# Kernel tuning notes

Measured on AMD Instinct MI355X. Metric: run time of the kernel, lower is better.

## Reference

```python
import jax, jax.numpy as jnp
import numpy as np

N_HEAD = 16
N_KV_HEADS = 4
HEAD_DIM = 64  # n_emb // n_head = 1024 // 16
WINDOW = 512
NEG_INF = float('-inf')


def _rope_tables(T, dim, dtype):
    inv_freq = 1.0 / (10000.0 ** (jnp.arange(0, dim, 2, dtype=jnp.float32) / dim))
    t = jnp.arange(T, dtype=jnp.float32)
    freqs = jnp.einsum('i,j->ij', t, inv_freq)          # [T, dim/2]
    emb = jnp.concatenate((freqs, freqs), axis=-1)       # [T, dim]
    return jnp.cos(emb).astype(dtype), jnp.sin(emb).astype(dtype)


def _apply_rope(x, cos, sin):
    # x: [B, H, T, D]; cos/sin: [T, D]
    x1, x2 = jnp.split(x, 2, axis=-1)
    x_rot = jnp.concatenate((-x2, x1), axis=-1)
    return x * cos + x_rot * sin


def setup_inputs() -> dict:
    key = jax.random.key(0)
    ks = jax.random.split(key, 5)
    B, T, C = 1, 4096, 1024
    kv_dim = N_KV_HEADS * HEAD_DIM
    s = 0.02
    return {
        'x': jax.random.normal(ks[0], (B, T, C), jnp.float32),
        'wq': jax.random.normal(ks[1], (C, C), jnp.float32) * s,
        'wk': jax.random.normal(ks[2], (kv_dim, C), jnp.float32) * s,
        'wv': jax.random.normal(ks[3], (kv_dim, C), jnp.float32) * s,
        'wo': jax.random.normal(ks[4], (C, C), jnp.float32) * s,
    }


def reference(x, wq, wk, wv, wo):
    B, T, C = x.shape
    n_rep = N_HEAD // N_KV_HEADS
    # QKV projections (torch Linear: x @ W.T)
    q = (x @ wq.T).reshape(B, T, N_HEAD, HEAD_DIM).transpose(0, 2, 1, 3)      # [B,H,T,D]
    k = (x @ wk.T).reshape(B, T, N_KV_HEADS, HEAD_DIM).transpose(0, 2, 1, 3)  # [B,Hkv,T,D]
    v = (x @ wv.T).reshape(B, T, N_KV_HEADS, HEAD_DIM).transpose(0, 2, 1, 3)
    # RoPE
    cos, sin = _rope_tables(T, HEAD_DIM, x.dtype)
    q = _apply_rope(q, cos, sin)
    k = _apply_rope(k, cos, sin)
    # GQA: repeat KV heads
    k = jnp.repeat(k, n_rep, axis=1)  # [B,H,T,D]
    v = jnp.repeat(v, n_rep, axis=1)
    # Sliding-window causal mask: allow j <= i and j > i - WINDOW
    i = jnp.arange(T)[:, None]
    j = jnp.arange(T)[None, :]
    allowed = (j <= i) & (j > i - WINDOW)  # [T,T]
    scale = 1.0 / np.sqrt(HEAD_DIM)
    scores = jnp.einsum('bhqd,bhkd->bhqk', q, k) * scale
    scores = jnp.where(allowed[None, None], scores, NEG_INF)
    attn = jax.nn.softmax(scores, axis=-1)
    y = jnp.einsum('bhqk,bhkd->bhqd', attn, v)            # [B,H,T,D]
    y = y.transpose(0, 2, 1, 3).reshape(B, T, C)
    return y @ wo.T
```

## Files before the change

kernel.cpp:

```cpp
#include <hip/hip_runtime.h>
#include <hip/hip_bf16.h>
#include <stdint.h>

#define T_SEQ 4096
#define CDIM  1024
#define NH    16
#define NKV   4
#define HD    64
#define WIN   512
#define KVD   256
#define QKVN  1536

typedef unsigned short ushort_t;
typedef __attribute__((ext_vector_type(8))) __bf16 bf16x8;
typedef __attribute__((ext_vector_type(4))) float  f32x4;
typedef __attribute__((ext_vector_type(4))) unsigned short us4;

__device__ inline unsigned short f2bf(float f) {
  unsigned u = __builtin_bit_cast(unsigned, f);
  u += 0x7fffu + ((u >> 16) & 1u);
  return (unsigned short)(u >> 16);
}

__device__ inline unsigned cvt_pk_bf16(float lo, float hi) {
  unsigned r;
  asm("v_cvt_pk_bf16_f32 %0, %1, %2" : "=v"(r) : "v"(lo), "v"(hi));
  return r;
}

__device__ inline f32x4 mfma16(bf16x8 a, bf16x8 b, f32x4 c) {
  return __builtin_amdgcn_mfma_f32_16x16x32_bf16(a, b, c, 0, 0, 0);
}

__device__ inline void load_lds16(const void* g, void* s) {
  __builtin_amdgcn_global_load_lds(
      (const __attribute__((address_space(1))) void*)g,
      (__attribute__((address_space(3))) void*)s, 16, 0, 0);
}

__global__ __launch_bounds__(256) void prep_kernel(
    const float* __restrict__ x,  const float* __restrict__ wq,
    const float* __restrict__ wk, const float* __restrict__ wv,
    const float* __restrict__ wo,
    ushort_t* __restrict__ xb, ushort_t* __restrict__ wqkvb,
    ushort_t* __restrict__ wob,
    float* __restrict__ ct, float* __restrict__ st) {
  const int NX  = T_SEQ * CDIM / 4;
  const int NWQ = CDIM * CDIM / 4;
  const int NWK = KVD * CDIM / 4;
  const int NCONV = NX + 2 * NWQ + 2 * NWK;
  int i = blockIdx.x * 256 + threadIdx.x;
  if (i >= NCONV) {
    int j = i - NCONV;
    if (j >= T_SEQ * 32) return;
    int t = j >> 5, f = j & 31;
    float inv = __builtin_exp2f(-(float)f * (13.287712379549449f / 32.0f));
    float a = (float)t * inv;
    ct[j] = cosf(a);
    st[j] = sinf(a);
    return;
  }
  const float4* src; ushort_t* dst; int off;
  if (i < NX)                        { src = (const float4*)x;  dst = xb;                              off = i; }
  else if (i < NX + NWQ)             { src = (const float4*)wq; dst = wqkvb;                           off = i - NX; }
  else if (i < NX + NWQ + NWK)       { src = (const float4*)wk; dst = wqkvb + CDIM * CDIM;             off = i - NX - NWQ; }
  else if (i < NX + NWQ + 2 * NWK)   { src = (const float4*)wv; dst = wqkvb + CDIM * CDIM + KVD * CDIM; off = i - NX - NWQ - NWK; }
  else                               { src = (const float4*)wo; dst = wob;                             off = i - NX - NWQ - 2 * NWK; }
  float4 v = src[off];
  us4 o; o.x = f2bf(v.x); o.y = f2bf(v.y); o.z = f2bf(v.z); o.w = f2bf(v.w);
  *(us4*)(dst + (size_t)off * 4) = o;
}

template <int EPI>
__global__ __launch_bounds__(256) void gemm_kernel(
    const ushort_t* __restrict__ A, const ushort_t* __restrict__ B, int K,
    float* __restrict__ outF,
    ushort_t* __restrict__ qbuf, ushort_t* __restrict__ kbuf, ushort_t* __restrict__ vt,
    const float* __restrict__ ct, const float* __restrict__ st) {
  __shared__ __align__(16) ushort_t smA[2][64 * 32];
  __shared__ __align__(16) ushort_t smB[2][128 * 32];
  const int tid = threadIdx.x, lane = tid & 63, wid = tid >> 6;

  const int id = blockIdx.x + (gridDim.x * blockIdx.y);
  const int nwg = gridDim.x * gridDim.y;
  const int swz = (id & 7) * (nwg >> 3) + (id >> 3);
  const int bm = (swz & 63) * 64, bn = (swz >> 6) * 128;

  const int wr = wid >> 1, wc = wid & 1;
  const int l15 = lane & 15, lg = lane >> 4;
  const int srow = lane >> 2;
  const int scol = (lane & 3) * 8;

  f32x4 acc[2][4];
#pragma unroll
  for (int i = 0; i < 2; i++)
#pragma unroll
    for (int j = 0; j < 4; j++) acc[i][j] = (f32x4)0.0f;

#define GSTAGE(buf, ktv)                                                                        \
  do {                                                                                          \
    load_lds16(A + (size_t)(bm + wid * 16 + srow) * K + (ktv) + scol, (char*)smA[buf] + wid * 1024);             \
    load_lds16(B + (size_t)(bn + wid * 16 + srow) * K + (ktv) + scol, (char*)smB[buf] + wid * 1024);             \
    load_lds16(B + (size_t)(bn + (wid + 4) * 16 + srow) * K + (ktv) + scol, (char*)smB[buf] + (wid + 4) * 1024); \
  } while (0)

  GSTAGE(0, 0);
  const int NK = K / 32;
  int cur = 0;
  for (int kt = 0; kt < NK; ++kt) {
    if (kt + 1 < NK) {
      GSTAGE(cur ^ 1, (kt + 1) * 32);
      asm volatile("s_waitcnt vmcnt(3)" ::: "memory");
    } else {
      asm volatile("s_waitcnt vmcnt(0)" ::: "memory");
    }
    __builtin_amdgcn_sched_barrier(0);
    __builtin_amdgcn_s_barrier();
    __builtin_amdgcn_sched_barrier(0);

    bf16x8 af[2], bfr[4];
#pragma unroll
    for (int mi = 0; mi < 2; mi++) af[mi] = *(const bf16x8*)&smA[cur][(wr * 32 + mi * 16 + l15) * 32 + lg * 8];
#pragma unroll
    for (int ni = 0; ni < 4; ni++) bfr[ni] = *(const bf16x8*)&smB[cur][(wc * 64 + ni * 16 + l15) * 32 + lg * 8];
#pragma unroll
    for (int mi = 0; mi < 2; mi++)
#pragma unroll
      for (int ni = 0; ni < 4; ni++) acc[mi][ni] = mfma16(af[mi], bfr[ni], acc[mi][ni]);

    __builtin_amdgcn_sched_barrier(0);
    __builtin_amdgcn_s_barrier();
    __builtin_amdgcn_sched_barrier(0);
    cur ^= 1;
  }
#undef GSTAGE

  const int col0 = bn + wc * 64;
  if (EPI == 1) {
#pragma unroll
    for (int mi = 0; mi < 2; mi++) {
      int r0 = bm + wr * 32 + mi * 16 + lg * 4;
#pragma unroll
      for (int ni = 0; ni < 4; ni++) {
        int c = col0 + ni * 16 + l15;
#pragma unroll
        for (int r = 0; r < 4; r++) outF[(size_t)(r0 + r) * CDIM + c] = acc[mi][ni][r];
      }
    }
  } else {
    if (col0 < CDIM + KVD) {
      bool isQ = (col0 < CDIM);
      ushort_t* obuf = isQ ? qbuf : kbuf;
      int ostride = isQ ? CDIM : KVD;
      int obase = isQ ? col0 : col0 - CDIM;
#pragma unroll
      for (int mi = 0; mi < 2; mi++) {
        int r0 = bm + wr * 32 + mi * 16 + lg * 4;
#pragma unroll
        for (int ni = 0; ni < 2; ni++) {
          int dd = ni * 16 + l15;
#pragma unroll
          for (int r = 0; r < 4; r++) {
            int t = r0 + r;
            float c_ = ct[t * 32 + dd], s_ = st[t * 32 + dd];
            float lo = acc[mi][ni][r], hi = acc[mi][ni + 2][r];
            obuf[(size_t)t * ostride + obase + dd]      = f2bf(lo * c_ - hi * s_);
            obuf[(size_t)t * ostride + obase + dd + 32] = f2bf(hi * c_ + lo * s_);
          }
        }
      }
    } else {
#pragma unroll
      for (int mi = 0; mi < 2; mi++) {
        int t0 = bm + wr * 32 + mi * 16 + lg * 4;
#pragma unroll
        for (int ni = 0; ni < 4; ni++) {
          int cv = col0 + ni * 16 + l15 - (CDIM + KVD);
          us4 o;
          o.x = f2bf(acc[mi][ni][0]); o.y = f2bf(acc[mi][ni][1]);
          o.z = f2bf(acc[mi][ni][2]); o.w = f2bf(acc[mi][ni][3]);
          *(us4*)&vt[(size_t)cv * T_SEQ + t0] = o;
        }
      }
    }
  }
}

__global__ __launch_bounds__(256) void attn_kernel(
    const ushort_t* __restrict__ qbuf, const ushort_t* __restrict__ kbuf,
    const ushort_t* __restrict__ vt, ushort_t* __restrict__ ybuf) {
  __shared__ __align__(16) ushort_t smK[2][64 * 64];
  __shared__ __align__(16) ushort_t smV[2][64 * 64];
  __shared__ __align__(16) ushort_t plds[4][32 * 64];
  const int tid = threadIdx.x, lane = tid & 63, wid = tid >> 6;
  const int l15 = lane & 15, lg = lane >> 4;
  const int blk = blockIdx.x;
  const int h  = (blk & 7) * 2 + ((blk >> 3) & 1);
  const int qb = (blk >> 4) * 128;
  const int kvh = h >> 2;
  const int qbw = qb + wid * 32;

  const int r8 = lane >> 3;
  const int cc = lane & 7;
  const int sc = ((cc ^ r8) * 8);
  const int ra = wid * 8 + r8;
  const int rb = (wid + 4) * 8 + r8;

  int kb0 = qb - (WIN - 1);
  if (kb0 < 0) kb0 = 0;
  kb0 &= ~63;
  const int nt = ((qb + 127) - kb0) / 64 + 1;

#define STAGE(buf, kbase)                                                                  \
  do {                                                                                     \
    load_lds16(kbuf + (size_t)((kbase) + ra) * KVD + kvh * HD + sc, (char*)smK[buf] + wid * 1024);        \
    load_lds16(kbuf + (size_t)((kbase) + rb) * KVD + kvh * HD + sc, (char*)smK[buf] + (wid + 4) * 1024);  \
    load_lds16(vt + (size_t)(kvh * HD + ra) * T_SEQ + (kbase) + sc, (char*)smV[buf] + wid * 1024);        \
    load_lds16(vt + (size_t)(kvh * HD + rb) * T_SEQ + (kbase) + sc, (char*)smV[buf] + (wid + 4) * 1024);  \
  } while (0)

  STAGE(0, kb0);

  bf16x8 qf[2][2];
#pragma unroll
  for (int h2 = 0; h2 < 2; h2++) {
    const ushort_t* qrow = qbuf + (size_t)(qbw + h2 * 16 + l15) * CDIM + h * HD;
    qf[h2][0] = *(const bf16x8*)(qrow + lg * 8);
    qf[h2][1] = *(const bf16x8*)(qrow + 32 + lg * 8);
  }

  f32x4 o[2][4];
#pragma unroll
  for (int i = 0; i < 2; i++)
#pragma unroll
    for (int j = 0; j < 4; j++) o[i][j] = (f32x4)0.f;
  float lpart[2] = {0.f, 0.f};
  const float SC = 0.125f * 1.4426950408889634f;
  ushort_t* pl = &plds[wid][0];
  const int sw = l15 & 7;
  const int pswz = sw << 4;

  int cur = 0;
  for (int t = 0; t < nt; ++t) {
    const int kb = kb0 + t * 64;
    if (t + 1 < nt) {
      STAGE(cur ^ 1, kb + 64);
      asm volatile("s_waitcnt vmcnt(4)" ::: "memory");
    } else {
      asm volatile("s_waitcnt vmcnt(0)" ::: "memory");
    }
    __builtin_amdgcn_sched_barrier(0);
    __builtin_amdgcn_s_barrier();
    __builtin_amdgcn_sched_barrier(0);

    if (kb <= qbw + 31) {
      const ushort_t* sk = smK[cur];
      const ushort_t* sv_ = smV[cur];

      bf16x8 kf[4][2];
#pragma unroll
      for (int g = 0; g < 4; g++) {
        kf[g][0] = *(const bf16x8*)&sk[(g * 16 + l15) * 64 + ((lg ^ sw) * 8)];
        kf[g][1] = *(const bf16x8*)&sk[(g * 16 + l15) * 64 + (((4 + lg) ^ sw) * 8)];
      }

      f32x4 s[2][4];
      __builtin_amdgcn_s_setprio(1);
#pragma unroll
      for (int h2 = 0; h2 < 2; h2++)
#pragma unroll
        for (int g = 0; g < 4; g++) {
          s[h2][g] = mfma16(kf[g][0], qf[h2][0], (f32x4)0.f);
          s[h2][g] = mfma16(kf[g][1], qf[h2][1], s[h2][g]);
        }
      __builtin_amdgcn_s_setprio(0);

      const bool nomask = (kb + 63 <= qbw) && (kb > qbw + 31 - WIN);
#pragma unroll
      for (int h2 = 0; h2 < 2; h2++) {
        const int q = qbw + h2 * 16 + l15;
        float ps = 0.f;
#pragma unroll
        for (int g = 0; g < 4; g++) {
          float p0, p1, p2, p3;
          if (nomask) {
            p0 = __builtin_exp2f(s[h2][g][0] * SC);
            p1 = __builtin_exp2f(s[h2][g][1] * SC);
            p2 = __builtin_exp2f(s[h2][g][2] * SC);
            p3 = __builtin_exp2f(s[h2][g][3] * SC);
          } else {
            int k0 = kb + g * 16 + lg * 4;
            p0 = __builtin_exp2f((k0 + 0 <= q && k0 + 0 > q - WIN) ? s[h2][g][0] * SC : -3e38f);
            p1 = __builtin_exp2f((k0 + 1 <= q && k0 + 1 > q - WIN) ? s[h2][g][1] * SC : -3e38f);
            p2 = __builtin_exp2f((k0 + 2 <= q && k0 + 2 > q - WIN) ? s[h2][g][2] * SC : -3e38f);
            p3 = __builtin_exp2f((k0 + 3 <= q && k0 + 3 > q - WIN) ? s[h2][g][3] * SC : -3e38f);
          }
          ps += (p0 + p1) + (p2 + p3);
          uint2 w;
          w.x = cvt_pk_bf16(p0, p1);
          w.y = cvt_pk_bf16(p2, p3);
          *(uint2*)((char*)pl + (h2 * 16 + l15) * 128 + ((g * 32 + lg * 8) ^ pswz)) = w;
        }
        lpart[h2] += ps;
      }

      asm volatile("s_waitcnt lgkmcnt(0)" ::: "memory");
      __builtin_amdgcn_sched_barrier(0);
      bf16x8 pf[2][2];
#pragma unroll
      for (int h2 = 0; h2 < 2; h2++) {
        pf[h2][0] = *(const bf16x8*)((const char*)pl + (h2 * 16 + l15) * 128 + ((lg * 16) ^ pswz));
        pf[h2][1] = *(const bf16x8*)((const char*)pl + (h2 * 16 + l15) * 128 + ((64 + lg * 16) ^ pswz));
      }

      __builtin_amdgcn_s_setprio(1);
#pragma unroll
      for (int n = 0; n < 4; n++) {
        bf16x8 v0 = *(const bf16x8*)&sv_[(n * 16 + l15) * 64 + ((lg ^ sw) * 8)];
        bf16x8 v1 = *(const bf16x8*)&sv_[(n * 16 + l15) * 64 + (((4 + lg) ^ sw) * 8)];
        o[0][n] = mfma16(pf[0][0], v0, o[0][n]);
        o[0][n] = mfma16(pf[0][1], v1, o[0][n]);
        o[1][n] = mfma16(pf[1][0], v0, o[1][n]);
        o[1][n] = mfma16(pf[1][1], v1, o[1][n]);
      }
      __builtin_amdgcn_s_setprio(0);
    }
    __builtin_amdgcn_sched_barrier(0);
    __builtin_amdgcn_s_barrier();
    __builtin_amdgcn_sched_barrier(0);
    cur ^= 1;
  }
#undef STAGE

#pragma unroll
  for (int h2 = 0; h2 < 2; h2++) {
    float l = lpart[h2];
    l += __shfl_xor(l, 16);
    l += __shfl_xor(l, 32);
    float inv = 1.f / l;
    float i0 = __shfl(inv, lg * 4 + 0);
    float i1 = __shfl(inv, lg * 4 + 1);
    float i2 = __shfl(inv, lg * 4 + 2);
    float i3 = __shfl(inv, lg * 4 + 3);
    ushort_t* yb = ybuf + (size_t)(qbw + h2 * 16) * CDIM + h * HD;
#pragma unroll
    for (int r = 0; r < 4; r++) {
      float ir = (r == 0) ? i0 : (r == 1) ? i1 : (r == 2) ? i2 : i3;
      size_t t = lg * 4 + r;
      yb[t * CDIM + 0  + l15] = f2bf(o[h2][0][r] * ir);
      yb[t * CDIM + 16 + l15] = f2bf(o[h2][1][r] * ir);
      yb[t * CDIM + 32 + l15] = f2bf(o[h2][2][r] * ir);
      yb[t * CDIM + 48 + l15] = f2bf(o[h2][3][r] * ir);
    }
  }
}

extern "C" void kernel_launch(void* const* d_in, const int* in_sizes, int n_in,
                              void* d_out, int out_size, void* d_ws, size_t ws_size,
                              hipStream_t stream) {
  const float* x  = (const float*)d_in[0];
  const float* wq = (const float*)d_in[1];
  const float* wk = (const float*)d_in[2];
  const float* wv = (const float*)d_in[3];
  const float* wo = (const float*)d_in[4];
  float* out = (float*)d_out;

  char* ws = (char*)d_ws;
  ushort_t* xb    = (ushort_t*)(ws + 0);
  ushort_t* wqkvb = (ushort_t*)(ws + 8388608);
  ushort_t* wob   = (ushort_t*)(ws + 11534336);
  ushort_t* qbuf  = (ushort_t*)(ws + 13631488);
  ushort_t* kbuf  = (ushort_t*)(ws + 22020096);
  ushort_t* vt    = (ushort_t*)(ws + 24117248);
  ushort_t* ybuf  = (ushort_t*)(ws + 26214400);
  float*    ct    = (float*)(ws + 34603008);
  float*    st    = (float*)(ws + 35127296);

  prep_kernel<<<7168, 256, 0, stream>>>(x, wq, wk, wv, wo, xb, wqkvb, wob, ct, st);

  dim3 g1(64, 12);
  gemm_kernel<0><<<g1, 256, 0, stream>>>(xb, wqkvb, CDIM, nullptr, qbuf, kbuf, vt, ct, st);

  attn_kernel<<<512, 256, 0, stream>>>(qbuf, kbuf, vt, ybuf);

  dim3 g2(64, 8);
  gemm_kernel<1><<<g2, 256, 0, stream>>>(ybuf, wob, CDIM, out, nullptr, nullptr, nullptr, nullptr, nullptr);
}
```

Before: 88.95 us.

## Halve attention query tile, transpose P in registers via permlane swaps

The attention kernel now gives each wave 16 query rows instead of 32, so each block covers 64 queries and the grid doubles to 1024 blocks, with launch bounds asking for 4 blocks per SM. The P matrix is no longer round-tripped through an LDS scratch buffer. Instead the packed bf16 probabilities are rearranged in registers with v_permlane32/16_swap to form the MFMA A operand. The intent is more parallelism and occupancy and less LDS traffic and synchronisation. In exchange, K/V tiles are loaded and staged more times per head, since each block reuses them over fewer queries.

After: 83.51 us. 6.1% less time.

```diff
diff --git a/kernel.cpp b/kernel.cpp
--- a/kernel.cpp
+++ b/kernel.cpp
@@ -186,19 +186,18 @@
   }
 }
 
-__global__ __launch_bounds__(256) void attn_kernel(
+__global__ __launch_bounds__(256, 4) void attn_kernel(
     const ushort_t* __restrict__ qbuf, const ushort_t* __restrict__ kbuf,
     const ushort_t* __restrict__ vt, ushort_t* __restrict__ ybuf) {
   __shared__ __align__(16) ushort_t smK[2][64 * 64];
   __shared__ __align__(16) ushort_t smV[2][64 * 64];
-  __shared__ __align__(16) ushort_t plds[4][32 * 64];
   const int tid = threadIdx.x, lane = tid & 63, wid = tid >> 6;
   const int l15 = lane & 15, lg = lane >> 4;
   const int blk = blockIdx.x;
   const int h  = (blk & 7) * 2 + ((blk >> 3) & 1);
-  const int qb = (blk >> 4) * 128;
+  const int qb = (blk >> 4) * 64;
   const int kvh = h >> 2;
-  const int qbw = qb + wid * 32;
+  const int qbw = qb + wid * 16;
 
   const int r8 = lane >> 3;
   const int cc = lane & 7;
@@ -209,7 +208,7 @@
   int kb0 = qb - (WIN - 1);
   if (kb0 < 0) kb0 = 0;
   kb0 &= ~63;
-  const int nt = ((qb + 127) - kb0) / 64 + 1;
+  const int nt = ((qb + 63) - kb0) / 64 + 1;
 
 #define STAGE(buf, kbase)                                                                  \
   do {                                                                                     \
@@ -221,24 +220,16 @@
 
   STAGE(0, kb0);
 
-  bf16x8 qf[2][2];
-#pragma unroll
-  for (int h2 = 0; h2 < 2; h2++) {
-    const ushort_t* qrow = qbuf + (size_t)(qbw + h2 * 16 + l15) * CDIM + h * HD;
-    qf[h2][0] = *(const bf16x8*)(qrow + lg * 8);
-    qf[h2][1] = *(const bf16x8*)(qrow + 32 + lg * 8);
-  }
-
-  f32x4 o[2][4];
-#pragma unroll
-  for (int i = 0; i < 2; i++)
-#pragma unroll
-    for (int j = 0; j < 4; j++) o[i][j] = (f32x4)0.f;
-  float lpart[2] = {0.f, 0.f};
+  const ushort_t* qrow = qbuf + (size_t)(qbw + l15) * CDIM + h * HD;
+  bf16x8 qf0 = *(const bf16x8*)(qrow + lg * 8);
+  bf16x8 qf1 = *(const bf16x8*)(qrow + 32 + lg * 8);
+
+  f32x4 o[4];
+#pragma unroll
+  for (int j = 0; j < 4; j++) o[j] = (f32x4)0.f;
+  float lpart = 0.f;
   const float SC = 0.125f * 1.4426950408889634f;
-  ushort_t* pl = &plds[wid][0];
   const int sw = l15 & 7;
-  const int pswz = sw << 4;
 
   int cur = 0;
   for (int t = 0; t < nt; ++t) {
@@ -253,64 +244,63 @@
     __builtin_amdgcn_s_barrier();
     __builtin_amdgcn_sched_barrier(0);
 
-    if (kb <= qbw + 31) {
+    if (kb <= qbw + 15) {
       const ushort_t* sk = smK[cur];
       const ushort_t* sv_ = smV[cur];
 
-      bf16x8 kf[4][2];
+      f32x4 s[4];
+      __builtin_amdgcn_s_setprio(1);
 #pragma unroll
       for (int g = 0; g < 4; g++) {
-        kf[g][0] = *(const bf16x8*)&sk[(g * 16 + l15) * 64 + ((lg ^ sw) * 8)];
-        kf[g][1] = *(const bf16x8*)&sk[(g * 16 + l15) * 64 + (((4 + lg) ^ sw) * 8)];
-      }
-
-      f32x4 s[2][4];
-      __builtin_amdgcn_s_setprio(1);
-#pragma unroll
-      for (int h2 = 0; h2 < 2; h2++)
-#pragma unroll
-        for (int g = 0; g < 4; g++) {
-          s[h2][g] = mfma16(kf[g][0], qf[h2][0], (f32x4)0.f);
-          s[h2][g] = mfma16(kf[g][1], qf[h2][1], s[h2][g]);
-        }
+        bf16x8 k0 = *(const bf16x8*)&sk[(g * 16 + l15) * 64 + ((lg ^ sw) * 8)];
+        bf16x8 k1 = *(const bf16x8*)&sk[(g * 16 + l15) * 64 + (((4 + lg) ^ sw) * 8)];
+        s[g] = mfma16(k0, qf0, (f32x4)0.f);
+        s[g] = mfma16(k1, qf1, s[g]);
+      }
       __builtin_amdgcn_s_setprio(0);
 
-      const bool nomask = (kb + 63 <= qbw) && (kb > qbw + 31 - WIN);
-#pragma unroll
-      for (int h2 = 0; h2 < 2; h2++) {
-        const int q = qbw + h2 * 16 + l15;
+      const bool nomask = (kb + 63 <= qbw) && (kb > qbw + 15 - WIN);
+      unsigned pw[8];
+      {
+        const int q = qbw + l15;
         float ps = 0.f;
 #pragma unroll
         for (int g = 0; g < 4; g++) {
           float p0, p1, p2, p3;
           if (nomask) {
-            p0 = __builtin_exp2f(s[h2][g][0] * SC);
-            p1 = __builtin_exp2f(s[h2][g][1] * SC);
-            p2 = __builtin_exp2f(s[h2][g][2] * SC);
-            p3 = __builtin_exp2f(s[h2][g][3] * SC);
+            p0 = __builtin_exp2f(s[g][0] * SC);
+            p1 = __builtin_exp2f(s[g][1] * SC);
+            p2 = __builtin_exp2f(s[g][2] * SC);
+            p3 = __builtin_exp2f(s[g][3] * SC);
           } else {
             int k0 = kb + g * 16 + lg * 4;
-            p0 = __builtin_exp2f((k0 + 0 <= q && k0 + 0 > q - WIN) ? s[h2][g][0] * SC : -3e38f);
-            p1 = __builtin_exp2f((k0 + 1 <= q && k0 + 1 > q - WIN) ? s[h2][g][1] * SC : -3e38f);
-            p2 = __builtin_exp2f((k0 + 2 <= q && k0 + 2 > q - WIN) ? s[h2][g][2] * SC : -3e38f);
-            p3 = __builtin_exp2f((k0 + 3 <= q && k0 + 3 > q - WIN) ? s[h2][g][3] * SC : -3e38f);
+            p0 = __builtin_exp2f((k0 + 0 <= q && k0 + 0 > q - WIN) ? s[g][0] * SC : -3e38f);
+            p1 = __builtin_exp2f((k0 + 1 <= q && k0 + 1 > q - WIN) ? s[g][1] * SC : -3e38f);
+            p2 = __builtin_exp2f((k0 + 2 <= q && k0 + 2 > q - WIN) ? s[g][2] * SC : -3e38f);
+            p3 = __builtin_exp2f((k0 + 3 <= q && k0 + 3 > q - WIN) ? s[g][3] * SC : -3e38f);
           }
           ps += (p0 + p1) + (p2 + p3);
-          uint2 w;
-          w.x = cvt_pk_bf16(p0, p1);
-          w.y = cvt_pk_bf16(p2, p3);
-          *(uint2*)((char*)pl + (h2 * 16 + l15) * 128 + ((g * 32 + lg * 8) ^ pswz)) = w;
+          pw[g * 2 + 0] = cvt_pk_bf16(p0, p1);
+          pw[g * 2 + 1] = cvt_pk_bf16(p2, p3);
         }
-        lpart[h2] += ps;
-      }
-
-      asm volatile("s_waitcnt lgkmcnt(0)" ::: "memory");
-      __builtin_amdgcn_sched_barrier(0);
-      bf16x8 pf[2][2];
-#pragma unroll
-      for (int h2 = 0; h2 < 2; h2++) {
-        pf[h2][0] = *(const bf16x8*)((const char*)pl + (h2 * 16 + l15) * 128 + ((lg * 16) ^ pswz));
-        pf[h2][1] = *(const bf16x8*)((const char*)pl + (h2 * 16 + l15) * 128 + ((64 + lg * 16) ^ pswz));
+        lpart += ps;
+      }
+
+      asm("v_permlane32_swap_b32 %0, %1" : "+v"(pw[0]), "+v"(pw[2]));
+      asm("v_permlane32_swap_b32 %0, %1" : "+v"(pw[1]), "+v"(pw[3]));
+      asm("v_permlane32_swap_b32 %0, %1" : "+v"(pw[4]), "+v"(pw[6]));
+      asm("v_permlane32_swap_b32 %0, %1" : "+v"(pw[5]), "+v"(pw[7]));
+      asm("v_permlane16_swap_b32 %0, %1" : "+v"(pw[0]), "+v"(pw[2]));
+      asm("v_permlane16_swap_b32 %0, %1" : "+v"(pw[1]), "+v"(pw[3]));
+      asm("v_permlane16_swap_b32 %0, %1" : "+v"(pw[4]), "+v"(pw[6]));
+      asm("v_permlane16_swap_b32 %0, %1" : "+v"(pw[5]), "+v"(pw[7]));
+      bf16x8 pf0, pf1;
+      {
+        union { unsigned u[4]; bf16x8 v; } c0, c1;
+        c0.u[0] = pw[0]; c0.u[1] = pw[1]; c0.u[2] = pw[2]; c0.u[3] = pw[3];
+        c1.u[0] = pw[4]; c1.u[1] = pw[5]; c1.u[2] = pw[6]; c1.u[3] = pw[7];
+        pf0 = c0.v;
+        pf1 = c1.v;
       }
 
       __builtin_amdgcn_s_setprio(1);
@@ -318,10 +308,8 @@
       for (int n = 0; n < 4; n++) {
         bf16x8 v0 = *(const bf16x8*)&sv_[(n * 16 + l15) * 64 + ((lg ^ sw) * 8)];
         bf16x8 v1 = *(const bf16x8*)&sv_[(n * 16 + l15) * 64 + (((4 + lg) ^ sw) * 8)];
-        o[0][n] = mfma16(pf[0][0], v0, o[0][n]);
-        o[0][n] = mfma16(pf[0][1], v1, o[0][n]);
-        o[1][n] = mfma16(pf[1][0], v0, o[1][n]);
-        o[1][n] = mfma16(pf[1][1], v1, o[1][n]);
+        o[n] = mfma16(pf0, v0, o[n]);
+        o[n] = mfma16(pf1, v1, o[n]);
       }
       __builtin_amdgcn_s_setprio(0);
     }
@@ -332,9 +320,8 @@
   }
 #undef STAGE
 
-#pragma unroll
-  for (int h2 = 0; h2 < 2; h2++) {
-    float l = lpart[h2];
+  {
+    float l = lpart;
     l += __shfl_xor(l, 16);
     l += __shfl_xor(l, 32);
     float inv = 1.f / l;
@@ -342,15 +329,15 @@
     float i1 = __shfl(inv, lg * 4 + 1);
     float i2 = __shfl(inv, lg * 4 + 2);
     float i3 = __shfl(inv, lg * 4 + 3);
-    ushort_t* yb = ybuf + (size_t)(qbw + h2 * 16) * CDIM + h * HD;
+    ushort_t* yb = ybuf + (size_t)qbw * CDIM + h * HD;
 #pragma unroll
     for (int r = 0; r < 4; r++) {
       float ir = (r == 0) ? i0 : (r == 1) ? i1 : (r == 2) ? i2 : i3;
       size_t t = lg * 4 + r;
-      yb[t * CDIM + 0  + l15] = f2bf(o[h2][0][r] * ir);
-      yb[t * CDIM + 16 + l15] = f2bf(o[h2][1][r] * ir);
-      yb[t * CDIM + 32 + l15] = f2bf(o[h2][2][r] * ir);
-      yb[t * CDIM + 48 + l15] = f2bf(o[h2][3][r] * ir);
+      yb[t * CDIM + 0  + l15] = f2bf(o[0][r] * ir);
+      yb[t * CDIM + 16 + l15] = f2bf(o[1][r] * ir);
+      yb[t * CDIM + 32 + l15] = f2bf(o[2][r] * ir);
+      yb[t * CDIM + 48 + l15] = f2bf(o[3][r] * ir);
     }
   }
 }
@@ -381,7 +368,7 @@
   dim3 g1(64, 12);
   gemm_kernel<0><<<g1, 256, 0, stream>>>(xb, wqkvb, CDIM, nullptr, qbuf, kbuf, vt, ct, st);
 
-  attn_kernel<<<512, 256, 0, stream>>>(qbuf, kbuf, vt, ybuf);
+  attn_kernel<<<1024, 256, 0, stream>>>(qbuf, kbuf, vt, ybuf);
 
   dim3 g2(64, 8);
   gemm_kernel<1><<<g2, 256, 0, stream>>>(ybuf, wob, CDIM, out, nullptr, nullptr, nullptr, nullptr, nullptr);
```
